# Kernel tuning notes

Hardware: AMD Instinct MI355X
Metric: run time of the kernel (lower is better)

## Reference

```python
import jax, jax.numpy as jnp
import numpy as np

B, S, HID = 2, 2048, 2048
HK, HV, DK, DV, K = 16, 32, 128, 128, 4
KEY_DIM, VAL_DIM = HK * DK, HV * DV      # 2048, 4096
CONV_DIM = 2 * KEY_DIM + VAL_DIM         # 8192
EPS = 1e-6


def setup_inputs() -> dict:
    key = jax.random.key(0)
    ks = jax.random.split(key, 8)
    s = 0.02
    return {
        "hidden_states": jax.random.normal(ks[0], (B, S, HID), jnp.float32),
        "W_qkvz": jax.random.normal(ks[1], (2 * KEY_DIM + 2 * VAL_DIM, HID), jnp.float32) * s,
        "W_ba": jax.random.normal(ks[2], (2 * HV, HID), jnp.float32) * s,
        "conv_w": jax.random.normal(ks[3], (CONV_DIM, 1, K), jnp.float32) * 0.1,
        "dt_bias": jnp.ones((HV,), jnp.float32),
        "A_log": jnp.log(jax.random.uniform(ks[4], (HV,), jnp.float32, 0.5, 8.0)),
        "norm_weight": jnp.ones((DV,), jnp.float32),
        "W_out": jax.random.normal(ks[5], (HID, VAL_DIM), jnp.float32) * s,
    }


def _split_qkvz_ba(qkvz, ba):
    # matches fix_query_key_value_ordering: per-k-head layout [q(dk), k(dk), v(r*dv), z(r*dv)]
    r = HV // HK
    qkvz = qkvz.reshape(B, S, HK, 2 * DK + 2 * r * DV)
    q = qkvz[..., :DK]
    k = qkvz[..., DK:2 * DK]
    v = qkvz[..., 2 * DK:2 * DK + r * DV].reshape(B, S, HV, DV)
    z = qkvz[..., 2 * DK + r * DV:].reshape(B, S, HV, DV)
    ba = ba.reshape(B, S, HK, 2 * r)
    b = ba[..., :r].reshape(B, S, HV)
    a = ba[..., r:].reshape(B, S, HV)
    return q, k, v, z, b, a


def _causal_conv(x, w):
    # x: (B,S,C), w: (C,1,K); depthwise, left-pad K-1 == torch pad=K-1 then truncate to S
    y = jax.lax.conv_general_dilated(
        x.transpose(0, 2, 1), w, (1,), [(K - 1, 0)],
        dimension_numbers=("NCH", "OIH", "NCH"), feature_group_count=CONV_DIM)
    return y.transpose(0, 2, 1)


def _l2norm(x):
    return x * jax.lax.rsqrt(jnp.sum(x * x, axis=-1, keepdims=True) + EPS)


def _gated_delta_rule(q, k, v, a, b, A_log, dt_bias):
    # q,k: (B,S,HK,DK); v: (B,S,HV,DV); a,b: (B,S,HV)
    r = HV // HK
    q = jnp.repeat(q, r, axis=2)   # (B,S,HV,DK), GQA expand
    k = jnp.repeat(k, r, axis=2)
    q = _l2norm(q) * (DK ** -0.5)
    k = _l2norm(k)
    g = -jnp.exp(A_log) * jax.nn.softplus(a + dt_bias)   # (B,S,HV), log-decay
    beta = jax.nn.sigmoid(b)

    qT = q.transpose(1, 0, 2, 3)   # (S,B,HV,DK)
    kT = k.transpose(1, 0, 2, 3)
    vT = v.transpose(1, 0, 2, 3)   # (S,B,HV,DV)
    gT = g.transpose(1, 0, 2)
    bT = beta.transpose(1, 0, 2)

    def step(Sst, inp):
        qt, kt, vt, gt, bt = inp
        Sst = Sst * jnp.exp(gt)[..., None, None]                  # per-head decay
        kv = jnp.einsum("bhk,bhkv->bhv", kt, Sst)                # retrieve memory
        delta = (vt - kv) * bt[..., None]                         # delta rule update
        Sst = Sst + jnp.einsum("bhk,bhv->bhkv", kt, delta)
        out = jnp.einsum("bhk,bhkv->bhv", qt, Sst)
        return Sst, out

    S0 = jnp.zeros((B, HV, DK, DV), q.dtype)
    _, o = jax.lax.scan(step, S0, (qT, kT, vT, gT, bT))
    return o.transpose(1, 0, 2, 3)   # (B,S,HV,DV)


def _rmsnorm_gated(x, w, gate):
    # norm(x) * w * silu(gate), norm before gate, over last dim
    var = jnp.mean(x * x, axis=-1, keepdims=True)
    return x * jax.lax.rsqrt(var + EPS) * w * jax.nn.silu(gate)


def reference(hidden_states, W_qkvz, W_ba, conv_w, dt_bias, A_log, norm_weight, W_out):
    qkvz = hidden_states @ W_qkvz.T            # (B,S,12288)
    ba = hidden_states @ W_ba.T                # (B,S,64)
    q, k, v, z, b, a = _split_qkvz_ba(qkvz, ba)
    mixed = jnp.concatenate([q.reshape(B, S, KEY_DIM),
                             k.reshape(B, S, KEY_DIM),
                             v.reshape(B, S, VAL_DIM)], axis=-1)
    mixed = jax.nn.silu(_causal_conv(mixed, conv_w))
    q = mixed[..., :KEY_DIM].reshape(B, S, HK, DK)
    k = mixed[..., KEY_DIM:2 * KEY_DIM].reshape(B, S, HK, DK)
    v = mixed[..., 2 * KEY_DIM:].reshape(B, S, HV, DV)
    core = _gated_delta_rule(q, k, v, a, b, A_log, dt_bias)   # (B,S,HV,DV)
    core = _rmsnorm_gated(core, norm_weight, z)
    return core.reshape(B, S, VAL_DIM) @ W_out.T
```

## Files before the change

kernel.cpp:

```cpp
#include <hip/hip_runtime.h>
#include <cstdint>
#include <cstddef>

#define B_ 2
#define S_ 2048
#define HID_ 2048
#define HK_ 16
#define HV_ 32
#define DK_ 128
#define DV_ 128
#define KEY_DIM_ 2048
#define VAL_DIM_ 4096
#define QKVZ_DIM_ 12288
#define BA_DIM_ 64
#define CONV_DIM_ 8192
#define EPS_ 1e-6f
#define NCHUNK_ 32
#define CL_ 64

typedef unsigned short bf16;
typedef __attribute__((ext_vector_type(8))) short bf16x8;
typedef __attribute__((ext_vector_type(8))) unsigned short u16x8;
typedef __attribute__((ext_vector_type(4))) float f32x4;

__device__ __forceinline__ float silu_f(float x) { return x / (1.f + expf(-x)); }

__device__ __forceinline__ bf16 f2bf(float x) {
    unsigned int u = __float_as_uint(x);
    u += 0x7FFF + ((u >> 16) & 1);
    return (bf16)(u >> 16);
}
__device__ __forceinline__ float bf2f(bf16 x) {
    return __uint_as_float((unsigned)x << 16);
}
#define BF2F_LO(u) __uint_as_float((unsigned)(u) << 16)
#define BF2F_HI(u) __uint_as_float((unsigned)(u) & 0xFFFF0000u)

__device__ __forceinline__ float bf_lane(const uint4& x, int j) {
    const unsigned wv = (&x.x)[j >> 1];
    return (j & 1) ? BF2F_HI(wv) : BF2F_LO(wv);
}

typedef const __attribute__((address_space(1))) unsigned int cgu32;
typedef __attribute__((address_space(3))) unsigned int lsu32;
__device__ __forceinline__ void gld16(const void* g, void* l) {
    __builtin_amdgcn_global_load_lds((cgu32*)g, (lsu32*)l, 16, 0, 0);
}

#define MFMA16(a, b, c) __builtin_amdgcn_mfma_f32_16x16x32_bf16((a), (b), (c), 0, 0, 0)

__global__ __launch_bounds__(256) void f2bf_kernel(const float* __restrict__ in,
                                                   bf16* __restrict__ out) {
    const int64_t i = (int64_t)blockIdx.x * 256 + threadIdx.x;
    const float4 v = ((const float4*)in)[i];
    ushort4 o;
    o.x = f2bf(v.x); o.y = f2bf(v.y); o.z = f2bf(v.z); o.w = f2bf(v.w);
    ((ushort4*)out)[i] = o;
}

template <int BNT, int OUTBF16>
__global__ __launch_bounds__(512, 2) void gemm256_nt(
    const bf16* __restrict__ A, const bf16* __restrict__ Bm,
    void* __restrict__ Cv, int M, int N, int K) {
    __shared__ bf16 ringA[3][8192];
    __shared__ bf16 ringB[3][BNT * 32];
    const int tid = threadIdx.x;
    const int w = tid >> 6;
    const int l = tid & 63;
    const int wm = w >> 2;
    const int wn = w & 3;
    const int fl = l & 15;
    const int fk = (l >> 4) * 8;
    const int bm = blockIdx.y, bn = blockIdx.x;

    const int srow = tid >> 2;
    const int scol = (((tid & 3) ^ ((tid >> 3) & 3)) << 3);
    const bf16* Ag0 = A + (size_t)(bm * 256 + srow) * K + scol;
    const bf16* Ag1 = A + (size_t)(bm * 256 + 128 + srow) * K + scol;
    const bf16* Bg0 = Bm + (size_t)(bn * BNT + srow) * K + scol;
    const bf16* Bg1 = Bm + (size_t)(bn * BNT + 128 + srow) * K + scol;

    const int kswz = fk ^ (((fl >> 1) & 3) << 3);
    const int NFR = BNT / 64;
    int aoff[8], boff[4];
#pragma unroll
    for (int mi = 0; mi < 8; ++mi)
        aoff[mi] = (wm * 128 + mi * 16 + fl) * 32 + kswz;
#pragma unroll
    for (int ni = 0; ni < NFR; ++ni)
        boff[ni] = (wn * (BNT / 4) + ni * 16 + fl) * 32 + kswz;

    f32x4 acc[8][4];
#pragma unroll
    for (int mi = 0; mi < 8; ++mi)
#pragma unroll
        for (int ni = 0; ni < NFR; ++ni) acc[mi][ni] = (f32x4){0.f, 0.f, 0.f, 0.f};

#define STAGEX(kt, slot)                                                       \
    do {                                                                       \
        const int _k = (kt) * 32;                                              \
        gld16(Ag0 + _k, &ringA[slot][w * 512]);                                \
        gld16(Ag1 + _k, &ringA[slot][4096 + w * 512]);                         \
        gld16(Bg0 + _k, &ringB[slot][w * 512]);                                \
        if (BNT == 256) gld16(Bg1 + _k, &ringB[slot][4096 + w * 512]);         \
    } while (0)

    const int nkt = K >> 5;
    STAGEX(0, 0);
    STAGEX(1, 1);

    for (int t = 0; t < nkt; ++t) {
        if (BNT == 256)
            asm volatile("s_waitcnt vmcnt(4)" ::: "memory");
        else
            asm volatile("s_waitcnt vmcnt(3)" ::: "memory");
        __builtin_amdgcn_s_barrier();
        __builtin_amdgcn_sched_barrier(0);
        const int slot = t % 3;
        const bf16* As_ = ringA[slot];
        const bf16* Bs_ = ringB[slot];
        bf16x8 af[8], bfr[4];
#pragma unroll
        for (int mi = 0; mi < 8; ++mi)
            af[mi] = *(const bf16x8*)(As_ + aoff[mi]);
#pragma unroll
        for (int ni = 0; ni < NFR; ++ni)
            bfr[ni] = *(const bf16x8*)(Bs_ + boff[ni]);
        const int kt2 = (t + 2 < nkt) ? (t + 2) : (nkt - 1);
        STAGEX(kt2, (t + 2) % 3);
        asm volatile("s_waitcnt lgkmcnt(0)" ::: "memory");
        __builtin_amdgcn_sched_barrier(0);
        __builtin_amdgcn_s_setprio(1);
#pragma unroll
        for (int mi = 0; mi < 8; ++mi)
#pragma unroll
            for (int ni = 0; ni < NFR; ++ni)
                acc[mi][ni] = MFMA16(af[mi], bfr[ni], acc[mi][ni]);
        __builtin_amdgcn_s_setprio(0);
    }
#undef STAGEX

#pragma unroll
    for (int mi = 0; mi < 8; ++mi)
#pragma unroll
        for (int ni = 0; ni < NFR; ++ni)
#pragma unroll
            for (int r = 0; r < 4; ++r) {
                const int row = bm * 256 + wm * 128 + mi * 16 + (l >> 4) * 4 + r;
                const int col = bn * BNT + wn * (BNT / 4) + ni * 16 + fl;
                if (OUTBF16)
                    ((bf16*)Cv)[(size_t)row * N + col] = f2bf(acc[mi][ni][r]);
                else
                    ((float*)Cv)[(size_t)row * N + col] = acc[mi][ni][r];
            }
}

#define BM 64
#define BN 64
#define BKK 32

__global__ __launch_bounds__(256) void gemm_ba_ksplit(
    const float* __restrict__ A, const float* __restrict__ Bm,
    float* __restrict__ Cpart) {
    __shared__ float As[BKK][BM + 4];
    __shared__ float Bs[BKK][BN + 4];
    const int tid = threadIdx.x;
    const int tx = tid & 15;
    const int ty = tid >> 4;
    const int ks = blockIdx.x;
    const int bm = blockIdx.y;
    const float* Ab = A + (size_t)bm * BM * HID_;
    const float* Bb = Bm;
    const int lr = tid >> 2;
    const int lc = (tid & 3) << 3;

    float c[4][4] = {{0.f, 0.f, 0.f, 0.f}, {0.f, 0.f, 0.f, 0.f},
                     {0.f, 0.f, 0.f, 0.f}, {0.f, 0.f, 0.f, 0.f}};

    const int kbeg = ks * 512;
    for (int k0 = kbeg; k0 < kbeg + 512; k0 += BKK) {
        const float4 a0 = *(const float4*)(Ab + (size_t)lr * HID_ + k0 + lc);
        const float4 a1 = *(const float4*)(Ab + (size_t)lr * HID_ + k0 + lc + 4);
        const float4 b0 = *(const float4*)(Bb + (size_t)lr * HID_ + k0 + lc);
        const float4 b1 = *(const float4*)(Bb + (size_t)lr * HID_ + k0 + lc + 4);
        __syncthreads();
        As[lc + 0][lr] = a0.x; As[lc + 1][lr] = a0.y;
        As[lc + 2][lr] = a0.z; As[lc + 3][lr] = a0.w;
        As[lc + 4][lr] = a1.x; As[lc + 5][lr] = a1.y;
        As[lc + 6][lr] = a1.z; As[lc + 7][lr] = a1.w;
        Bs[lc + 0][lr] = b0.x; Bs[lc + 1][lr] = b0.y;
        Bs[lc + 2][lr] = b0.z; Bs[lc + 3][lr] = b0.w;
        Bs[lc + 4][lr] = b1.x; Bs[lc + 5][lr] = b1.y;
        Bs[lc + 6][lr] = b1.z; Bs[lc + 7][lr] = b1.w;
        __syncthreads();
#pragma unroll
        for (int kk = 0; kk < BKK; ++kk) {
            const float4 Av = *(const float4*)&As[kk][ty << 2];
            const float4 Bv = *(const float4*)&Bs[kk][tx << 2];
            const float aa[4] = {Av.x, Av.y, Av.z, Av.w};
            const float bb[4] = {Bv.x, Bv.y, Bv.z, Bv.w};
#pragma unroll
            for (int i = 0; i < 4; ++i)
#pragma unroll
                for (int j = 0; j < 4; ++j)
                    c[i][j] = fmaf(aa[i], bb[j], c[i][j]);
        }
    }
    float* Cp = Cpart + (size_t)ks * ((size_t)B_ * S_ * 64) +
                (size_t)(bm * BM + (ty << 2)) * 64 + (tx << 2);
#pragma unroll
    for (int i = 0; i < 4; ++i)
        *(float4*)(Cp + (size_t)i * 64) =
            make_float4(c[i][0], c[i][1], c[i][2], c[i][3]);
}

__global__ __launch_bounds__(256) void conv_silu_kernel(
    const bf16* __restrict__ qkvz, const float* __restrict__ cw,
    bf16* __restrict__ qbf, bf16* __restrict__ kbf, bf16* __restrict__ vbuf,
    bf16* __restrict__ zbuf) {
    const int64_t idx = (int64_t)blockIdx.x * 256 + threadIdx.x;
    const int cg = (int)(idx % 1536);
    const int64_t bs = idx / 1536;
    const int s = (int)(bs & (S_ - 1));
    const int c0 = cg << 3;

    int col;
    bf16* outp;
    if (c0 < KEY_DIM_) {
        col = ((c0 >> 7) * 768) + (c0 & 127);
        outp = qbf + bs * KEY_DIM_ + c0;
    } else if (c0 < 2 * KEY_DIM_) {
        const int c2 = c0 - KEY_DIM_;
        col = ((c2 >> 7) * 768) + 128 + (c2 & 127);
        outp = kbf + bs * KEY_DIM_ + c2;
    } else if (c0 < 2 * KEY_DIM_ + VAL_DIM_) {
        const int c3 = c0 - 2 * KEY_DIM_;
        col = ((c3 >> 8) * 768) + 256 + (c3 & 255);
        outp = vbuf + bs * VAL_DIM_ + c3;
    } else {
        const int zc = c0 - (2 * KEY_DIM_ + VAL_DIM_);
        const int hv = zc >> 7;
        col = (hv >> 1) * 768 + 512 + (hv & 1) * 128 + (zc & 127);
        outp = zbuf + bs * VAL_DIM_ + zc;
    }
    const bf16* xp = qkvz + bs * (int64_t)QKVZ_DIM_ + col;
    if (c0 >= 2 * KEY_DIM_ + VAL_DIM_) {
        *(uint4*)outp = *(const uint4*)xp;
        return;
    }
    const uint4 zero4 = {0u, 0u, 0u, 0u};
    const uint4 x0 = *(const uint4*)xp;
    const uint4 x1 = (s >= 1) ? *(const uint4*)(xp - QKVZ_DIM_) : zero4;
    const uint4 x2 = (s >= 2) ? *(const uint4*)(xp - 2 * QKVZ_DIM_) : zero4;
    const uint4 x3 = (s >= 3) ? *(const uint4*)(xp - 3 * QKVZ_DIM_) : zero4;
    u16x8 o;
#pragma unroll
    for (int j = 0; j < 8; ++j) {
        const float4 wv = *(const float4*)(cw + (size_t)(c0 + j) * 4);
        float acc = wv.w * bf_lane(x0, j);
        acc = fmaf(wv.z, bf_lane(x1, j), acc);
        acc = fmaf(wv.y, bf_lane(x2, j), acc);
        acc = fmaf(wv.x, bf_lane(x3, j), acc);
        o[j] = f2bf(silu_f(acc));
    }
    *(u16x8*)outp = o;
}

__global__ __launch_bounds__(256) void normalize_qk_kernel(
    bf16* __restrict__ qbf, bf16* __restrict__ kbf) {
    const int wid = (blockIdx.x * 256 + threadIdx.x) >> 6;
    const int lane = threadIdx.x & 63;
    const int hk = wid & (HK_ - 1);
    const int64_t bs = wid >> 4;
    bf16* qp = qbf + bs * KEY_DIM_ + hk * DK_ + lane * 2;
    bf16* kp = kbf + bs * KEY_DIM_ + hk * DK_ + lane * 2;
    const ushort2 qw = *(const ushort2*)qp;
    const ushort2 kw = *(const ushort2*)kp;
    const float q0 = bf2f(qw.x), q1 = bf2f(qw.y);
    const float k0 = bf2f(kw.x), k1 = bf2f(kw.y);
    float qs = fmaf(q0, q0, q1 * q1);
    float ks = fmaf(k0, k0, k1 * k1);
#pragma unroll
    for (int m = 1; m < 64; m <<= 1) {
        qs += __shfl_xor(qs, m);
        ks += __shfl_xor(ks, m);
    }
    const float qsc = rsqrtf(qs + EPS_) * 0.08838834764831845f;
    const float ksc = rsqrtf(ks + EPS_);
    ushort2 oq, ok;
    oq.x = f2bf(q0 * qsc); oq.y = f2bf(q1 * qsc);
    ok.x = f2bf(k0 * ksc); ok.y = f2bf(k1 * ksc);
    *(ushort2*)qp = oq;
    *(ushort2*)kp = ok;
}

__global__ __launch_bounds__(256) void gate_kernel(
    const float* __restrict__ ba_part, const float* __restrict__ A_log,
    const float* __restrict__ dt_bias, float* __restrict__ gbuf,
    float* __restrict__ betabuf) {
    const int idx = blockIdx.x * 256 + threadIdx.x;
    const int hv = idx & (HV_ - 1);
    const int bs = idx >> 5;
    const int hk = hv >> 1, j = hv & 1;
    const size_t SP = (size_t)B_ * S_ * 64;
    const float* p = ba_part + (size_t)bs * 64 + hk * 4;
    const float bval = p[j] + p[SP + j] + p[2 * SP + j] + p[3 * SP + j];
    const float aval =
        p[2 + j] + p[SP + 2 + j] + p[2 * SP + 2 + j] + p[3 * SP + 2 + j];
    const float x = aval + dt_bias[hv];
    const float sp = (x > 20.f) ? x : log1pf(expf(x));
    gbuf[idx] = -expf(A_log[hv]) * sp;
    betabuf[idx] = 1.f / (1.f + expf(-bval));
}

__global__ __launch_bounds__(256) void p1_kernel(
    const bf16* __restrict__ qbf, const bf16* __restrict__ kbf,
    const bf16* __restrict__ vbuf, const float* __restrict__ gbuf,
    const float* __restrict__ betabuf, bf16* __restrict__ WkA,
    bf16* __restrict__ QgA, bf16* __restrict__ Kg2A, bf16* __restrict__ UA,
    bf16* __restrict__ LA, float* __restrict__ gcArr) {
    const int ch = blockIdx.x;
    const int bh = ch >> 5, c = ch & 31;
    const int b = bh >> 5, hv = bh & 31;
    const int hk = hv >> 1;
    const int tid = threadIdx.x;
    const int w = tid >> 6, l = tid & 63;
    const int fl = l & 15, fk = (l >> 4) * 8;

    __shared__ float Gls[CL_];
    __shared__ float Bls[CL_];
    __shared__ float Egt[CL_];
    __shared__ float Egc[CL_];
    __shared__ float A_ls[CL_][CL_ + 1];
    __shared__ bf16 Tbf[CL_ * CL_];
    __shared__ bf16 Vt[128 * 72];
    __shared__ bf16 Kt[128 * 72];

    if (tid < 64) {
        float G = gbuf[((size_t)(b * S_ + c * 64 + tid)) * HV_ + hv];
        Bls[tid] = betabuf[((size_t)(b * S_ + c * 64 + tid)) * HV_ + hv];
#pragma unroll
        for (int d = 1; d < 64; d <<= 1) {
            const float n = __shfl_up(G, d, 64);
            if (tid >= d) G += n;
        }
        Gls[tid] = G;
        const float eg = expf(G);
        Egt[tid] = eg;
        Egc[tid] = expf(__shfl(G, 63, 64) - G);
        if (tid == 63) gcArr[ch] = eg;
    }
    __syncthreads();

    const bf16* kc = kbf + ((size_t)(b * S_ + c * 64)) * KEY_DIM_ + hk * DK_;
    const bf16* qc = qbf + ((size_t)(b * S_ + c * 64)) * KEY_DIM_ + hk * DK_;
    bf16* LC = LA + (size_t)ch * 4096;

    f32x4 accK[4], accQ[4];
#pragma unroll
    for (int n = 0; n < 4; ++n) {
        accK[n] = (f32x4){0.f, 0.f, 0.f, 0.f};
        accQ[n] = (f32x4){0.f, 0.f, 0.f, 0.f};
    }
#pragma unroll
    for (int kk = 0; kk < 4; ++kk) {
        const bf16x8 aK =
            *(const bf16x8*)(kc + (size_t)(w * 16 + fl) * KEY_DIM_ + fk + 32 * kk);
        const bf16x8 aQ =
            *(const bf16x8*)(qc + (size_t)(w * 16 + fl) * KEY_DIM_ + fk + 32 * kk);
#pragma unroll
        for (int n = 0; n < 4; ++n) {
            const bf16x8 bK = *(const bf16x8*)(kc + (size_t)(n * 16 + fl) * KEY_DIM_ +
                                               fk + 32 * kk);
            accK[n] = MFMA16(aK, bK, accK[n]);
            accQ[n] = MFMA16(aQ, bK, accQ[n]);
        }
    }
#pragma unroll
    for (int n = 0; n < 4; ++n)
#pragma unroll
        for (int r = 0; r < 4; ++r) {
            const int t = w * 16 + (l >> 4) * 4 + r;
            const int s = n * 16 + fl;
            const float eg = expf(Gls[t] - Gls[s]);
            A_ls[t][s] = (s < t) ? Bls[t] * eg * accK[n][r] : 0.f;
            const float lv = (s <= t) ? eg * accQ[n][r] : 0.f;
            LC[t * 64 + s] = f2bf(lv);
        }
    __syncthreads();

    bf16* QgC = QgA + (size_t)ch * 8192;
    bf16* KgC = Kg2A + (size_t)ch * 8192;

    if (w == 0) {
        float Tcol[64];
#pragma unroll
        for (int t = 0; t < 64; ++t) {
            float acc = (t == l) ? 1.f : 0.f;
#pragma unroll
            for (int s = 0; s < t; ++s)
                acc = fmaf(-A_ls[t][s], Tcol[s], acc);
            Tcol[t] = acc;
            Tbf[t * 64 + l] = f2bf(acc);
        }
    } else if (w == 1) {
        for (int i = l; i < 8192; i += 64) {
            const int d = i & 127, s = i >> 7;
            Vt[d * 72 + s] = f2bf(
                bf2f(vbuf[((size_t)(b * S_ + c * 64 + s)) * VAL_DIM_ + hv * DV_ + d]) *
                Bls[s]);
        }
    } else if (w == 2) {
        for (int i = l; i < 8192; i += 64) {
            const int d = i & 127, s = i >> 7;
            Kt[d * 72 + s] =
                f2bf(bf2f(kc[(size_t)s * KEY_DIM_ + d]) * Bls[s] * Egt[s]);
        }
    } else {
        for (int i = l; i < 8192; i += 64) {
            const int d = i & 127, t = i >> 7;
            QgC[t * 128 + d] = f2bf(bf2f(qc[(size_t)t * KEY_DIM_ + d]) * Egt[t]);
            KgC[d * 64 + t] = f2bf(bf2f(kc[(size_t)t * KEY_DIM_ + d]) * Egc[t]);
        }
    }
    __syncthreads();

    bf16* UC = UA + (size_t)ch * 8192;
    bf16* WkC = WkA + (size_t)ch * 8192;
    f32x4 accU[8], accW[8];
#pragma unroll
    for (int n = 0; n < 8; ++n) {
        accU[n] = (f32x4){0.f, 0.f, 0.f, 0.f};
        accW[n] = (f32x4){0.f, 0.f, 0.f, 0.f};
    }
#pragma unroll
    for (int kk = 0; kk < 2; ++kk) {
        const bf16x8 aT = *(const bf16x8*)(Tbf + (w * 16 + fl) * 64 + fk + 32 * kk);
#pragma unroll
        for (int n = 0; n < 8; ++n) {
            const bf16x8 bV = *(const bf16x8*)(Vt + (n * 16 + fl) * 72 + fk + 32 * kk);
            const bf16x8 bK2 = *(const bf16x8*)(Kt + (n * 16 + fl) * 72 + fk + 32 * kk);
            accU[n] = MFMA16(aT, bV, accU[n]);
            accW[n] = MFMA16(aT, bK2, accW[n]);
        }
    }
#pragma unroll
    for (int n = 0; n < 8; ++n)
#pragma unroll
        for (int r = 0; r < 4; ++r) {
            const int t = w * 16 + (l >> 4) * 4 + r;
            const int col = n * 16 + fl;
            UC[t * 128 + col] = f2bf(accU[n][r]);
            WkC[t * 128 + col] = f2bf(accW[n][r]);
        }
}

__global__ __launch_bounds__(256) void p2_kernel(
    const bf16* __restrict__ WkA, const bf16* __restrict__ QgA,
    const bf16* __restrict__ Kg2A, const bf16* __restrict__ UA,
    const bf16* __restrict__ LA, const float* __restrict__ gcArr,
    bf16* __restrict__ core) {
    const int xcd = blockIdx.x & 7;
    const int rr = blockIdx.x >> 3;
    const int bh = xcd * 8 + (rr & 7);
    const int dvb = rr >> 3;
    const int b = bh >> 5, hv = bh & 31;
    const int tid = threadIdx.x;
    const int w = tid >> 6, l = tid & 63;
    const int fl = l & 15, fk = (l >> 4) * 8;

    __shared__ bf16 Sbf[32 * 136];
    __shared__ bf16 Dbf[32 * 72];

    for (int i = tid; i < 32 * 136; i += 256) Sbf[i] = 0;
    f32x4 accS[2][2];
#pragma unroll
    for (int m = 0; m < 2; ++m)
#pragma unroll
        for (int n = 0; n < 2; ++n) accS[m][n] = (f32x4){0.f, 0.f, 0.f, 0.f};
    __syncthreads();

    for (int c = 0; c < NCHUNK_; ++c) {
        const size_t ch = (size_t)bh * 32 + c;
        const bf16* WkC = WkA + ch * 8192;
        const bf16* QgC = QgA + ch * 8192;
        const bf16* KgC = Kg2A + ch * 8192;
        const bf16* UC = UA + ch * 8192;
        const bf16* LC = LA + ch * 4096;

        f32x4 accD[2], accO[2];
#pragma unroll
        for (int n = 0; n < 2; ++n) {
            accD[n] = (f32x4){0.f, 0.f, 0.f, 0.f};
            accO[n] = (f32x4){0.f, 0.f, 0.f, 0.f};
        }
#pragma unroll
        for (int kk = 0; kk < 4; ++kk) {
            const bf16x8 bS0 = *(const bf16x8*)(Sbf + (0 * 16 + fl) * 136 + fk + 32 * kk);
            const bf16x8 bS1 = *(const bf16x8*)(Sbf + (1 * 16 + fl) * 136 + fk + 32 * kk);
            const bf16x8 aW = *(const bf16x8*)(WkC + (w * 16 + fl) * 128 + fk + 32 * kk);
            const bf16x8 aQ = *(const bf16x8*)(QgC + (w * 16 + fl) * 128 + fk + 32 * kk);
            accD[0] = MFMA16(aW, bS0, accD[0]);
            accD[1] = MFMA16(aW, bS1, accD[1]);
            accO[0] = MFMA16(aQ, bS0, accO[0]);
            accO[1] = MFMA16(aQ, bS1, accO[1]);
        }
#pragma unroll
        for (int n = 0; n < 2; ++n)
#pragma unroll
            for (int r = 0; r < 4; ++r) {
                const int t = w * 16 + (l >> 4) * 4 + r;
                const int dvl = n * 16 + fl;
                const float u = bf2f(UC[t * 128 + dvb * 32 + dvl]);
                Dbf[dvl * 72 + t] = f2bf(u - accD[n][r]);
            }
        __syncthreads();

#pragma unroll
        for (int kk = 0; kk < 2; ++kk) {
            const bf16x8 bD0 = *(const bf16x8*)(Dbf + (0 * 16 + fl) * 72 + fk + 32 * kk);
            const bf16x8 bD1 = *(const bf16x8*)(Dbf + (1 * 16 + fl) * 72 + fk + 32 * kk);
            const bf16x8 aL = *(const bf16x8*)(LC + (w * 16 + fl) * 64 + fk + 32 * kk);
            accO[0] = MFMA16(aL, bD0, accO[0]);
            accO[1] = MFMA16(aL, bD1, accO[1]);
        }
#pragma unroll
        for (int n = 0; n < 2; ++n)
#pragma unroll
            for (int r = 0; r < 4; ++r) {
                const int t = w * 16 + (l >> 4) * 4 + r;
                const int col = hv * 128 + dvb * 32 + n * 16 + fl;
                core[((size_t)(b * S_ + c * 64 + t)) * VAL_DIM_ + col] =
                    f2bf(accO[n][r]);
            }

        const float gc = gcArr[ch];
#pragma unroll
        for (int m = 0; m < 2; ++m)
#pragma unroll
            for (int n = 0; n < 2; ++n)
#pragma unroll
                for (int r = 0; r < 4; ++r) accS[m][n][r] *= gc;
#pragma unroll
        for (int kk = 0; kk < 2; ++kk) {
            const bf16x8 bD0 = *(const bf16x8*)(Dbf + (0 * 16 + fl) * 72 + fk + 32 * kk);
            const bf16x8 bD1 = *(const bf16x8*)(Dbf + (1 * 16 + fl) * 72 + fk + 32 * kk);
#pragma unroll
            for (int m = 0; m < 2; ++m) {
                const bf16x8 aK =
                    *(const bf16x8*)(KgC + ((2 * w + m) * 16 + fl) * 64 + fk + 32 * kk);
                accS[m][0] = MFMA16(aK, bD0, accS[m][0]);
                accS[m][1] = MFMA16(aK, bD1, accS[m][1]);
            }
        }
        __syncthreads();
#pragma unroll
        for (int m = 0; m < 2; ++m)
#pragma unroll
            for (int n = 0; n < 2; ++n)
#pragma unroll
                for (int r = 0; r < 4; ++r) {
                    const int dk = (2 * w + m) * 16 + (l >> 4) * 4 + r;
                    const int dvl = n * 16 + fl;
                    Sbf[dvl * 136 + dk] = f2bf(accS[m][n][r]);
                }
        __syncthreads();
    }
}

__global__ __launch_bounds__(256) void rmsnorm_gate_kernel(
    bf16* __restrict__ core, const bf16* __restrict__ zbuf,
    const float* __restrict__ nw) {
    const int wid = (blockIdx.x * 256 + threadIdx.x) >> 6;
    const int lane = threadIdx.x & 63;
    const int hv = wid & (HV_ - 1);
    const int64_t bs = wid >> 5;
    bf16* x = core + (size_t)bs * VAL_DIM_ + hv * DV_;
    const float x0 = bf2f(x[lane]);
    const float x1 = bf2f(x[lane + 64]);
    float ss = fmaf(x0, x0, x1 * x1);
#pragma unroll
    for (int m = 1; m < 64; m <<= 1) ss += __shfl_xor(ss, m);
    const float inv = rsqrtf(ss * (1.f / 128.f) + EPS_);
    const bf16* z = zbuf + (size_t)bs * VAL_DIM_ + hv * DV_;
    x[lane] = f2bf(x0 * inv * nw[lane] * silu_f(bf2f(z[lane])));
    x[lane + 64] =
        f2bf(x1 * inv * nw[lane + 64] * silu_f(bf2f(z[lane + 64])));
}

extern "C" void kernel_launch(void* const* d_in, const int* in_sizes, int n_in,
                              void* d_out, int out_size, void* d_ws,
                              size_t ws_size, hipStream_t stream) {
    const float* hidden  = (const float*)d_in[0];
    const float* W_qkvz  = (const float*)d_in[1];
    const float* W_ba    = (const float*)d_in[2];
    const float* conv_w  = (const float*)d_in[3];
    const float* dt_bias = (const float*)d_in[4];
    const float* A_log   = (const float*)d_in[5];
    const float* norm_w  = (const float*)d_in[6];
    const float* W_out   = (const float*)d_in[7];
    float* out = (float*)d_out;

    bf16* R = (bf16*)d_ws;
    bf16* hidden_bf = R;
    bf16* Wq_bf = R + (size_t)8388608;
    bf16* qkvz  = R + (size_t)33554432;
    bf16* WkA  = R;
    bf16* QgA  = R + (size_t)16777216;
    bf16* Kg2A = R + (size_t)33554432;
    bf16* UA   = R + (size_t)50331648;
    bf16* LA   = R + (size_t)67108864;
    bf16* Wo_bf = R + (size_t)83886080;
    bf16* qbf   = Wo_bf + (size_t)8388608;
    bf16* kbf   = qbf + (size_t)8388608;
    bf16* vbuf  = kbf + (size_t)8388608;
    bf16* zbuf  = vbuf + (size_t)16777216;
    bf16* core  = zbuf + (size_t)16777216;
    float* ba_part = (float*)(core + (size_t)16777216);
    float* gbuf    = ba_part + 1048576;
    float* betabuf = gbuf + 131072;
    float* gcArr   = betabuf + 131072;

    const int MBS = B_ * S_;

    f2bf_kernel<<<8388608 / 1024, 256, 0, stream>>>(hidden, hidden_bf);
    f2bf_kernel<<<25165824 / 1024, 256, 0, stream>>>(W_qkvz, Wq_bf);
    f2bf_kernel<<<8388608 / 1024, 256, 0, stream>>>(W_out, Wo_bf);

    gemm256_nt<256, 1><<<dim3(QKVZ_DIM_ / 256, MBS / 256), 512, 0, stream>>>(
        hidden_bf, Wq_bf, (void*)qkvz, MBS, QKVZ_DIM_, HID_);
    gemm_ba_ksplit<<<dim3(4, 64), 256, 0, stream>>>(hidden, W_ba, ba_part);
    gate_kernel<<<(MBS * HV_) / 256, 256, 0, stream>>>(ba_part, A_log, dt_bias,
                                                       gbuf, betabuf);
    conv_silu_kernel<<<(int)(((int64_t)MBS * 1536) / 256), 256, 0, stream>>>(
        qkvz, conv_w, qbf, kbf, vbuf, zbuf);
    normalize_qk_kernel<<<(MBS * HK_ * 64) / 256, 256, 0, stream>>>(qbf, kbf);
    p1_kernel<<<2048, 256, 0, stream>>>(qbf, kbf, vbuf, gbuf, betabuf, WkA,
                                        QgA, Kg2A, UA, LA, gcArr);
    p2_kernel<<<256, 256, 0, stream>>>(WkA, QgA, Kg2A, UA, LA, gcArr, core);
    rmsnorm_gate_kernel<<<(MBS * HV_ * 64) / 256, 256, 0, stream>>>(core, zbuf,
                                                                    norm_w);
    gemm256_nt<128, 0><<<dim3(HID_ / 128, MBS / 256), 512, 0, stream>>>(
        core, Wo_bf, (void*)out, MBS, HID_, VAL_DIM_);
}
```

Measured before the change: 740.9 us.

## Fuse q/k L2 norm into conv kernel, merge casts, drop GEMM LDS wait

After: 711.4 us. 4.0% less time.

```diff
diff --git a/kernel.cpp b/kernel.cpp
--- a/kernel.cpp
+++ b/kernel.cpp
@@ -49,13 +49,39 @@
 
 #define MFMA16(a, b, c) __builtin_amdgcn_mfma_f32_16x16x32_bf16((a), (b), (c), 0, 0, 0)
 
-__global__ __launch_bounds__(256) void f2bf_kernel(const float* __restrict__ in,
-                                                   bf16* __restrict__ out) {
+template <int CTRL>
+__device__ __forceinline__ float dpp_ror_add(float x) {
+    const int t =
+        __builtin_amdgcn_update_dpp(0, __float_as_int(x), CTRL, 0xF, 0xF, false);
+    return x + __int_as_float(t);
+}
+__device__ __forceinline__ float row16_sum(float x) {
+    x = dpp_ror_add<0x128>(x);
+    x = dpp_ror_add<0x124>(x);
+    x = dpp_ror_add<0x122>(x);
+    x = dpp_ror_add<0x121>(x);
+    return x;
+}
+
+__global__ __launch_bounds__(256) void f2bf3_kernel(
+    const float* __restrict__ s0, const float* __restrict__ s1,
+    const float* __restrict__ s2, bf16* __restrict__ d0,
+    bf16* __restrict__ d1, bf16* __restrict__ d2) {
     const int64_t i = (int64_t)blockIdx.x * 256 + threadIdx.x;
-    const float4 v = ((const float4*)in)[i];
+    const float* src;
+    bf16* dst;
+    int64_t j;
+    if (i < 2097152) {
+        src = s0; dst = d0; j = i;
+    } else if (i < 2097152 + 6291456) {
+        src = s1; dst = d1; j = i - 2097152;
+    } else {
+        src = s2; dst = d2; j = i - (2097152 + 6291456);
+    }
+    const float4 v = ((const float4*)src)[j];
     ushort4 o;
     o.x = f2bf(v.x); o.y = f2bf(v.y); o.z = f2bf(v.z); o.w = f2bf(v.w);
-    ((ushort4*)out)[i] = o;
+    ((ushort4*)dst)[j] = o;
 }
 
 template <int BNT, int OUTBF16>
@@ -128,8 +154,6 @@
             bfr[ni] = *(const bf16x8*)(Bs_ + boff[ni]);
         const int kt2 = (t + 2 < nkt) ? (t + 2) : (nkt - 1);
         STAGEX(kt2, (t + 2) % 3);
-        asm volatile("s_waitcnt lgkmcnt(0)" ::: "memory");
-        __builtin_amdgcn_sched_barrier(0);
         __builtin_amdgcn_s_setprio(1);
 #pragma unroll
         for (int mi = 0; mi < 8; ++mi)
@@ -253,7 +277,7 @@
     const uint4 x1 = (s >= 1) ? *(const uint4*)(xp - QKVZ_DIM_) : zero4;
     const uint4 x2 = (s >= 2) ? *(const uint4*)(xp - 2 * QKVZ_DIM_) : zero4;
     const uint4 x3 = (s >= 3) ? *(const uint4*)(xp - 3 * QKVZ_DIM_) : zero4;
-    u16x8 o;
+    float y[8];
 #pragma unroll
     for (int j = 0; j < 8; ++j) {
         const float4 wv = *(const float4*)(cw + (size_t)(c0 + j) * 4);
@@ -261,37 +285,21 @@
         acc = fmaf(wv.z, bf_lane(x1, j), acc);
         acc = fmaf(wv.y, bf_lane(x2, j), acc);
         acc = fmaf(wv.x, bf_lane(x3, j), acc);
-        o[j] = f2bf(silu_f(acc));
-    }
+        y[j] = silu_f(acc);
+    }
+    float sc = 1.f;
+    if (c0 < 2 * KEY_DIM_) {
+        float ss = 0.f;
+#pragma unroll
+        for (int j = 0; j < 8; ++j) ss = fmaf(y[j], y[j], ss);
+        ss = row16_sum(ss);
+        sc = rsqrtf(ss + EPS_);
+        if (c0 < KEY_DIM_) sc *= 0.08838834764831845f;
+    }
+    u16x8 o;
+#pragma unroll
+    for (int j = 0; j < 8; ++j) o[j] = f2bf(y[j] * sc);
     *(u16x8*)outp = o;
-}
-
-__global__ __launch_bounds__(256) void normalize_qk_kernel(
-    bf16* __restrict__ qbf, bf16* __restrict__ kbf) {
-    const int wid = (blockIdx.x * 256 + threadIdx.x) >> 6;
-    const int lane = threadIdx.x & 63;
-    const int hk = wid & (HK_ - 1);
-    const int64_t bs = wid >> 4;
-    bf16* qp = qbf + bs * KEY_DIM_ + hk * DK_ + lane * 2;
-    bf16* kp = kbf + bs * KEY_DIM_ + hk * DK_ + lane * 2;
-    const ushort2 qw = *(const ushort2*)qp;
-    const ushort2 kw = *(const ushort2*)kp;
-    const float q0 = bf2f(qw.x), q1 = bf2f(qw.y);
-    const float k0 = bf2f(kw.x), k1 = bf2f(kw.y);
-    float qs = fmaf(q0, q0, q1 * q1);
-    float ks = fmaf(k0, k0, k1 * k1);
-#pragma unroll
-    for (int m = 1; m < 64; m <<= 1) {
-        qs += __shfl_xor(qs, m);
-        ks += __shfl_xor(ks, m);
-    }
-    const float qsc = rsqrtf(qs + EPS_) * 0.08838834764831845f;
-    const float ksc = rsqrtf(ks + EPS_);
-    ushort2 oq, ok;
-    oq.x = f2bf(q0 * qsc); oq.y = f2bf(q1 * qsc);
-    ok.x = f2bf(k0 * ksc); ok.y = f2bf(k1 * ksc);
-    *(ushort2*)qp = oq;
-    *(ushort2*)kp = ok;
 }
 
 __global__ __launch_bounds__(256) void gate_kernel(
@@ -623,9 +631,8 @@
 
     const int MBS = B_ * S_;
 
-    f2bf_kernel<<<8388608 / 1024, 256, 0, stream>>>(hidden, hidden_bf);
-    f2bf_kernel<<<25165824 / 1024, 256, 0, stream>>>(W_qkvz, Wq_bf);
-    f2bf_kernel<<<8388608 / 1024, 256, 0, stream>>>(W_out, Wo_bf);
+    f2bf3_kernel<<<40960, 256, 0, stream>>>(hidden, W_qkvz, W_out, hidden_bf,
+                                            Wq_bf, Wo_bf);
 
     gemm256_nt<256, 1><<<dim3(QKVZ_DIM_ / 256, MBS / 256), 512, 0, stream>>>(
         hidden_bf, Wq_bf, (void*)qkvz, MBS, QKVZ_DIM_, HID_);
@@ -634,7 +641,6 @@
                                                        gbuf, betabuf);
     conv_silu_kernel<<<(int)(((int64_t)MBS * 1536) / 256), 256, 0, stream>>>(
         qkvz, conv_w, qbf, kbf, vbuf, zbuf);
-    normalize_qk_kernel<<<(MBS * HK_ * 64) / 256, 256, 0, stream>>>(qbf, kbf);
     p1_kernel<<<2048, 256, 0, stream>>>(qbf, kbf, vbuf, gbuf, betabuf, WkA,
                                         QgA, Kg2A, UA, LA, gcArr);
     p2_kernel<<<256, 256, 0, stream>>>(WkA, QgA, Kg2A, UA, LA, gcArr, core);
```
